# Kernel optimization log

Measured on AMD Instinct MI355X. Metric: run time of the kernel, lower is better.

Reference implementation:

```python
import jax, jax.numpy as jnp
import numpy as np

T_HORIZON, S_DIM, A_DIM, H = 65536, 128, 8, 256
GAMMA, LMBDA, EPS_CLIP, VF_COEF, ENT_COEF = 0.99, 0.95, 0.2, 0.5, 0.01
LOG2PI = float(np.log(2.0 * np.pi))


def setup_inputs() -> dict:
    key = jax.random.key(0)
    ks = jax.random.split(key, 24)
    s = jax.random.normal(ks[0], (T_HORIZON, S_DIM), jnp.float32)
    a = jax.random.normal(ks[1], (T_HORIZON, A_DIM), jnp.float32)
    r = jax.random.normal(ks[2], (T_HORIZON, 1), jnp.float32)
    sp = jax.random.normal(ks[3], (T_HORIZON, S_DIM), jnp.float32)
    log_prob_a_old = jax.random.normal(ks[4], (T_HORIZON, 1), jnp.float32)
    d_mask = (jax.random.uniform(ks[5], (T_HORIZON, 1)) > 0.05).astype(jnp.float32)

    def lin(k, fan_in, fan_out, std):
        return jax.random.normal(k, (fan_in, fan_out), jnp.float32) * (std / np.sqrt(fan_in))

    params = dict(
        pi_W1=lin(ks[6], S_DIM, H, np.sqrt(2)), pi_b1=jnp.zeros((H,), jnp.float32),
        pi_W2=lin(ks[7], H, H, np.sqrt(2)),     pi_b2=jnp.zeros((H,), jnp.float32),
        mu_W=lin(ks[8], H, A_DIM, 0.01),        mu_b=jnp.zeros((A_DIM,), jnp.float32),
        log_std=jnp.zeros((A_DIM,), jnp.float32),
        v_W1=lin(ks[9], S_DIM, H, np.sqrt(2)),  v_b1=jnp.zeros((H,), jnp.float32),
        v_W2=lin(ks[10], H, H, np.sqrt(2)),     v_b2=jnp.zeros((H,), jnp.float32),
        vh_W=lin(ks[11], H, 1, 1.0),            vh_b=jnp.zeros((1,), jnp.float32),
    )
    return dict(s=s, a=a, r=r, sp=sp, log_prob_a_old=log_prob_a_old, d_mask=d_mask, **params)


def reference(s, a, r, sp, log_prob_a_old, d_mask,
              pi_W1, pi_b1, pi_W2, pi_b2, mu_W, mu_b, log_std,
              v_W1, v_b1, v_W2, v_b2, vh_W, vh_b):
    def mlp(x, W1, b1, W2, b2):
        return jnp.tanh(jnp.tanh(x @ W1 + b1) @ W2 + b2)

    def v_fn(x):
        return mlp(x, v_W1, v_b1, v_W2, v_b2) @ vh_W + vh_b  # [N, 1]

    # ---- GAE (computed under no_grad in the original) ----
    values = jax.lax.stop_gradient(v_fn(s))                  # [T, 1]
    v_last = jax.lax.stop_gradient(v_fn(sp[-1:]))            # [1, 1]
    next_values = jnp.concatenate([values[1:], v_last], axis=0)
    deltas = r + GAMMA * next_values * d_mask - values       # [T, 1]

    def gae_step(gae, inp):
        delta, m = inp
        gae = delta + GAMMA * LMBDA * m * gae
        return gae, gae

    _, advantages = jax.lax.scan(gae_step, jnp.zeros((1,), deltas.dtype),
                                 (deltas, d_mask), reverse=True)  # [T, 1]
    returns = advantages + values
    advantages = (advantages - advantages.mean()) / (advantages.std(ddof=1) + 1e-8)
    advantages = jax.lax.stop_gradient(advantages)
    returns = jax.lax.stop_gradient(returns)

    # ---- PPO clipped loss (single full-batch pass) ----
    mu = mlp(s, pi_W1, pi_b1, pi_W2, pi_b2) @ mu_W + mu_b    # [T, A]
    std = jnp.exp(log_std)
    log_prob = (-0.5 * ((a - mu) / std) ** 2 - log_std - 0.5 * LOG2PI).sum(-1, keepdims=True)
    ratio = jnp.exp(log_prob - log_prob_a_old)               # [T, 1]
    pg_loss = -jnp.minimum(ratio * advantages,
                           jnp.clip(ratio, 1.0 - EPS_CLIP, 1.0 + EPS_CLIP) * advantages).mean()
    diff = v_fn(s) - returns
    vf_loss = jnp.where(jnp.abs(diff) < 1.0, 0.5 * diff ** 2, jnp.abs(diff) - 0.5).mean()
    entropy = (0.5 + 0.5 * LOG2PI + log_std).mean()          # Normal entropy, constant over batch
    return pg_loss + VF_COEF * vf_loss - ENT_COEF * entropy
```

## Files before the change

### kernel.cpp

```cpp
#include <hip/hip_runtime.h>
#include <math.h>

#define TH 65536
#define SD 128
#define AD 8
#define HD 256

constexpr float GAMMA  = 0.99f;
constexpr float LMBDA  = 0.95f;
constexpr float EPSC   = 0.2f;
constexpr float VFC    = 0.5f;
constexpr float ENTC   = 0.01f;
constexpr float LOG2PI = 1.8378770664093453f;

typedef _Float16 half8 __attribute__((ext_vector_type(8)));
typedef __fp16 fp16x2 __attribute__((ext_vector_type(2)));
typedef __attribute__((ext_vector_type(4))) float f32x4;

constexpr size_t WS_VALUES = 0;
constexpr size_t WS_RATIO  = 131080;
constexpr size_t WS_CHP    = 196616;
constexpr size_t WS_CHB    = 196680;
constexpr size_t WS_SCAL   = 196744;
constexpr size_t WS_BF     = 196752;
constexpr size_t SW_PIW1 = 0;
constexpr size_t SW_PIW2 = 32768;
constexpr size_t SW_VW1  = 98304;
constexpr size_t SW_VW2  = 131072;

__device__ __forceinline__ unsigned pk2h(float a, float b) {
    fp16x2 h = __builtin_amdgcn_cvt_pkrtz(a, b);
    return __builtin_bit_cast(unsigned, h);
}

__device__ __forceinline__ float ftanh(float x) {
    float cx = fminf(fmaxf(x, -9.f), 9.f);
    float e = __expf(cx + cx);
    return (e - 1.f) * __builtin_amdgcn_rcpf(e + 1.f);
}

__global__ __launch_bounds__(256) void swizzle_kernel(
    const float* __restrict__ piW1, const float* __restrict__ vW1,
    const float* __restrict__ piW2, const float* __restrict__ vW2,
    unsigned short* __restrict__ dPiW1, unsigned short* __restrict__ dVW1,
    unsigned short* __restrict__ dPiW2, unsigned short* __restrict__ dVW2,
    float* __restrict__ scal)
{
    if (blockIdx.x == 0 && threadIdx.x < 8) scal[threadIdx.x] = 0.f;
    int g = blockIdx.x * 256 + threadIdx.x;
    const float* S; unsigned short* D; int lo;
    if      (g <  8192) { S = piW1; D = dPiW1; lo = 0;     }
    else if (g < 24576) { S = piW2; D = dPiW2; lo = 8192;  }
    else if (g < 32768) { S = vW1;  D = dVW1;  lo = 24576; }
    else                { S = vW2;  D = dVW2;  lo = 32768; }
    int q = g - lo;
    int k = q >> 6, n4 = (q & 63) * 4;
    float4 v = *(const float4*)(S + (size_t)k * HD + n4);
    int ks = k >> 5, kq = (k >> 3) & 3, j = k & 7;
    int nt = n4 >> 4, nr = n4 & 15;
    unsigned short* base = D + ((size_t)(ks * 16 + nt) * 64 + kq * 16 + nr) * 8 + j;
    unsigned p01 = pk2h(v.x, v.y);
    unsigned p23 = pk2h(v.z, v.w);
    base[0]  = (unsigned short)(p01 & 0xffff);
    base[8]  = (unsigned short)(p01 >> 16);
    base[16] = (unsigned short)(p23 & 0xffff);
    base[24] = (unsigned short)(p23 >> 16);
}

__device__ __forceinline__ void runlayer1(
    f32x4* acc, const unsigned short* __restrict__ Ws,
    const half8* afr, int colhalf, int lane)
{
#pragma unroll
    for (int nt = 0; nt < 8; ++nt) acc[nt] = (f32x4){0.f, 0.f, 0.f, 0.f};
#pragma unroll
    for (int ks = 0; ks < 4; ++ks) {
#pragma unroll
        for (int ntl = 0; ntl < 8; ++ntl) {
            half8 bf = ((const half8*)Ws)[(ks * 16 + colhalf * 8 + ntl) * 64 + lane];
            acc[ntl] = __builtin_amdgcn_mfma_f32_16x16x32_f16(afr[ks], bf, acc[ntl], 0, 0, 0);
        }
    }
}

__device__ __forceinline__ void runlayer2(
    f32x4* acc, const unsigned short* __restrict__ Ws,
    const unsigned short* h1, int l15, int quad, int rowgrp, int colhalf, int lane)
{
#pragma unroll
    for (int nt = 0; nt < 8; ++nt) acc[nt] = (f32x4){0.f, 0.f, 0.f, 0.f};
#pragma unroll
    for (int ks = 0; ks < 8; ++ks) {
        half8 af = *(const half8*)(h1 + (rowgrp * 16 + l15) * 264 + ks * 32 + quad * 8);
#pragma unroll
        for (int ntl = 0; ntl < 8; ++ntl) {
            half8 bf = ((const half8*)Ws)[(ks * 16 + colhalf * 8 + ntl) * 64 + lane];
            acc[ntl] = __builtin_amdgcn_mfma_f32_16x16x32_f16(af, bf, acc[ntl], 0, 0, 0);
        }
    }
}

__device__ __forceinline__ void store4(unsigned short* dst, int stride,
                                       float t0, float t1, float t2, float t3)
{
    unsigned p01 = pk2h(t0, t1), p23 = pk2h(t2, t3);
    dst[0]          = (unsigned short)(p01 & 0xffff);
    dst[stride]     = (unsigned short)(p01 >> 16);
    dst[2 * stride] = (unsigned short)(p23 & 0xffff);
    dst[3 * stride] = (unsigned short)(p23 >> 16);
}

__global__ __launch_bounds__(256, 4) void mlp_fused_kernel(
    const float* __restrict__ X, const float* __restrict__ Xlast,
    const unsigned short* __restrict__ piW1s, const float* __restrict__ pib1,
    const unsigned short* __restrict__ piW2s, const float* __restrict__ pib2,
    const float* __restrict__ muW, const float* __restrict__ mub,
    const float* __restrict__ logstd,
    const float* __restrict__ act, const float* __restrict__ lpold,
    const unsigned short* __restrict__ vW1s, const float* __restrict__ vb1,
    const unsigned short* __restrict__ vW2s, const float* __restrict__ vb2,
    const float* __restrict__ vhW, const float* __restrict__ vhb,
    float* __restrict__ values, float* __restrict__ ratio)
{
    __shared__ unsigned short h1[32 * 264];
    __shared__ float cmb[32 * 8];
    __shared__ float val[32];
    const int tid = threadIdx.x;
    const int lane = tid & 63, wave = tid >> 6;
    const int l15 = lane & 15, quad = lane >> 4;
    const int rowgrp = wave >> 1, colhalf = wave & 1;
    const bool vonly = (blockIdx.x == gridDim.x - 1);
    const float* Xp = vonly ? Xlast : X + (size_t)blockIdx.x * 32 * SD;
    const int nrows = vonly ? 1 : 32;
    const int vout0 = vonly ? TH : blockIdx.x * 32;

    if (tid < 32) val[tid] = 0.f;
    cmb[tid] = 0.f;

    const int rr = rowgrp * 16 + l15;
    const float* xrow = Xp + (size_t)(rr < nrows ? rr : 0) * SD;
    half8 afr[4];
#pragma unroll
    for (int ks = 0; ks < 4; ++ks) {
        float4 v0 = *(const float4*)(xrow + ks * 32 + quad * 8);
        float4 v1 = *(const float4*)(xrow + ks * 32 + quad * 8 + 4);
        if (rr >= nrows) { v0 = make_float4(0.f, 0.f, 0.f, 0.f); v1 = v0; }
        uint4 u = make_uint4(pk2h(v0.x, v0.y), pk2h(v0.z, v0.w),
                             pk2h(v1.x, v1.y), pk2h(v1.z, v1.w));
        afr[ks] = __builtin_bit_cast(half8, u);
    }

    f32x4 acc[8];

    if (!vonly) {
        runlayer1(acc, piW1s, afr, colhalf, lane);
#pragma unroll
        for (int ntl = 0; ntl < 8; ++ntl) {
            int col = (colhalf * 8 + ntl) * 16 + l15;
            float bb = pib1[col];
            store4(&h1[(rowgrp * 16 + quad * 4) * 264 + col], 264,
                   ftanh(acc[ntl][0] + bb), ftanh(acc[ntl][1] + bb),
                   ftanh(acc[ntl][2] + bb), ftanh(acc[ntl][3] + bb));
        }
        __syncthreads();
        runlayer2(acc, piW2s, h1, l15, quad, rowgrp, colhalf, lane);
        float pm[4][8];
#pragma unroll
        for (int rg = 0; rg < 4; ++rg)
#pragma unroll
            for (int aj = 0; aj < 8; ++aj) pm[rg][aj] = 0.f;
#pragma unroll
        for (int ntl = 0; ntl < 8; ++ntl) {
            int col = (colhalf * 8 + ntl) * 16 + l15;
            float bb = pib2[col];
            float4 w0 = *(const float4*)(muW + (size_t)col * AD);
            float4 w1 = *(const float4*)(muW + (size_t)col * AD + 4);
            float wv[8] = {w0.x, w0.y, w0.z, w0.w, w1.x, w1.y, w1.z, w1.w};
#pragma unroll
            for (int rg = 0; rg < 4; ++rg) {
                float hv = ftanh(acc[ntl][rg] + bb);
#pragma unroll
                for (int aj = 0; aj < 8; ++aj) pm[rg][aj] = fmaf(hv, wv[aj], pm[rg][aj]);
            }
        }
#pragma unroll
        for (int off = 8; off >= 1; off >>= 1)
#pragma unroll
            for (int rg = 0; rg < 4; ++rg)
#pragma unroll
                for (int aj = 0; aj < 8; ++aj)
                    pm[rg][aj] += __shfl_xor(pm[rg][aj], off, 16);
        if (l15 == 0) {
#pragma unroll
            for (int rg = 0; rg < 4; ++rg) {
                int rowi = rowgrp * 16 + quad * 4 + rg;
#pragma unroll
                for (int aj = 0; aj < 8; ++aj)
                    atomicAdd(&cmb[rowi * 8 + aj], pm[rg][aj]);
            }
        }
        __syncthreads();
        if (tid < 32) {
            int row = blockIdx.x * 32 + tid;
            const float* ar = act + (size_t)row * AD;
            float lp = 0.f;
#pragma unroll
            for (int aj = 0; aj < 8; ++aj) {
                float ls = logstd[aj];
                float mu = cmb[tid * 8 + aj] + mub[aj];
                float z = (ar[aj] - mu) * __expf(-ls);
                lp += -0.5f * z * z - ls;
            }
            lp -= 4.f * LOG2PI;
            ratio[row] = __expf(lp - lpold[row]);
        }
        __syncthreads();
    }

    runlayer1(acc, vW1s, afr, colhalf, lane);
#pragma unroll
    for (int ntl = 0; ntl < 8; ++ntl) {
        int col = (colhalf * 8 + ntl) * 16 + l15;
        float bb = vb1[col];
        store4(&h1[(rowgrp * 16 + quad * 4) * 264 + col], 264,
               ftanh(acc[ntl][0] + bb), ftanh(acc[ntl][1] + bb),
               ftanh(acc[ntl][2] + bb), ftanh(acc[ntl][3] + bb));
    }
    __syncthreads();
    runlayer2(acc, vW2s, h1, l15, quad, rowgrp, colhalf, lane);
    float vp[4] = {0.f, 0.f, 0.f, 0.f};
#pragma unroll
    for (int ntl = 0; ntl < 8; ++ntl) {
        int col = (colhalf * 8 + ntl) * 16 + l15;
        float bb = vb2[col], w = vhW[col];
#pragma unroll
        for (int rg = 0; rg < 4; ++rg) vp[rg] += ftanh(acc[ntl][rg] + bb) * w;
    }
#pragma unroll
    for (int off = 8; off >= 1; off >>= 1)
#pragma unroll
        for (int rg = 0; rg < 4; ++rg) vp[rg] += __shfl_xor(vp[rg], off, 16);
    if (l15 == 0) {
#pragma unroll
        for (int rg = 0; rg < 4; ++rg)
            atomicAdd(&val[rowgrp * 16 + quad * 4 + rg], vp[rg]);
    }
    __syncthreads();
    if (tid < nrows)
        values[vout0 + tid] = val[tid] + vhb[0];
}

__global__ __launch_bounds__(256) void gae_fused_kernel(
    const float* __restrict__ rw, const float* __restrict__ m,
    const float* __restrict__ values, const float* __restrict__ ratio,
    const float* __restrict__ logstd,
    float* __restrict__ chunkP, float* __restrict__ chunkB,
    float* __restrict__ scal, float* __restrict__ out)
{
    __shared__ float sp_[256], sb_[256];
    __shared__ float cp[64], cb[64];
    __shared__ float red[12];
    __shared__ float bcast[4];
    const int j = threadIdx.x;
    const int t0 = blockIdx.x * 1024 + j * 4;
    const float g = GAMMA * LMBDA;

    float4 vv = *(const float4*)(values + t0);
    float v4 = values[t0 + 4];
    float4 rr = *(const float4*)(rw + t0);
    float4 mm = *(const float4*)(m + t0);
    float vs[5] = {vv.x, vv.y, vv.z, vv.w, v4};
    float rs[4] = {rr.x, rr.y, rr.z, rr.w};
    float ms[4] = {mm.x, mm.y, mm.z, mm.w};
    float ds[4];
#pragma unroll
    for (int i = 0; i < 4; ++i)
        ds[i] = rs[i] + GAMMA * vs[i + 1] * ms[i] - vs[i];

    float P = 1.f, B = 0.f;
#pragma unroll
    for (int i = 3; i >= 0; --i) {
        float p = g * ms[i];
        B = ds[i] + p * B;
        P = p * P;
    }
    sp_[j] = P; sb_[j] = B;
    __syncthreads();
    for (int dstep = 1; dstep < 256; dstep <<= 1) {
        float pj = sp_[j], bj = sb_[j], pk = 1.f, bk = 0.f;
        if (j + dstep < 256) { pk = sp_[j + dstep]; bk = sb_[j + dstep]; }
        __syncthreads();
        sp_[j] = pj * pk;
        sb_[j] = bj + pj * bk;
        __syncthreads();
    }
    if (j == 0) {
        atomicExch(&chunkP[blockIdx.x], sp_[0]);
        atomicExch(&chunkB[blockIdx.x], sb_[0]);
        __threadfence();
        atomicAdd(&scal[5], 1.f);
        while (atomicAdd(&scal[5], 0.f) < 64.f) __builtin_amdgcn_s_sleep(2);
    }
    __syncthreads();
    if (j < 64) {
        cp[j] = atomicAdd(&chunkP[j], 0.f);
        cb[j] = atomicAdd(&chunkB[j], 0.f);
    }
    __syncthreads();
    if (j == 0) {
        float A = 0.f;
        for (int c = 63; c > (int)blockIdx.x; --c) A = cb[c] + cp[c] * A;
        bcast[0] = A;
    }
    __syncthreads();
    const float carry = bcast[0];

    float Pe = 1.f, Be = 0.f;
    if (j < 255) { Pe = sp_[j + 1]; Be = sb_[j + 1]; }
    float A = Be + Pe * carry;
    float s1 = 0.f, s2 = 0.f, vf = 0.f;
    float a4[4];
#pragma unroll
    for (int i = 3; i >= 0; --i) {
        A = ds[i] + g * ms[i] * A;
        a4[i] = A;
        float ab = fabsf(A);
        vf += (ab < 1.f) ? 0.5f * A * A : ab - 0.5f;
        s1 += A;
        s2 += A * A;
    }
#pragma unroll
    for (int off = 32; off >= 1; off >>= 1) {
        s1 += __shfl_down(s1, off, 64);
        s2 += __shfl_down(s2, off, 64);
        vf += __shfl_down(vf, off, 64);
    }
    if ((j & 63) == 0) {
        int w = j >> 6;
        red[w] = s1; red[4 + w] = s2; red[8 + w] = vf;
    }
    __syncthreads();
    if (j == 0) {
        atomicAdd(&scal[0], red[0] + red[1] + red[2] + red[3]);
        atomicAdd(&scal[1], red[4] + red[5] + red[6] + red[7]);
        atomicAdd(&scal[2], red[8] + red[9] + red[10] + red[11]);
        __threadfence();
        atomicAdd(&scal[6], 1.f);
        while (atomicAdd(&scal[6], 0.f) < 64.f) __builtin_amdgcn_s_sleep(2);
        bcast[1] = atomicAdd(&scal[0], 0.f);
        bcast[2] = atomicAdd(&scal[1], 0.f);
    }
    __syncthreads();

    const float ssum = bcast[1], ssq = bcast[2];
    const float meanA = ssum / (float)TH;
    const float varA = fmaxf((ssq - ssum * ssum / (float)TH) / (float)(TH - 1), 0.f);
    const float inv = 1.f / (sqrtf(varA) + 1e-8f);

    float4 r4 = *(const float4*)(ratio + t0);
    float rt[4] = {r4.x, r4.y, r4.z, r4.w};
    float pg = 0.f;
#pragma unroll
    for (int i = 0; i < 4; ++i) {
        float aN = (a4[i] - meanA) * inv;
        float rc = fminf(fmaxf(rt[i], 1.f - EPSC), 1.f + EPSC);
        pg -= fminf(rt[i] * aN, rc * aN);
    }
#pragma unroll
    for (int off = 32; off >= 1; off >>= 1) pg += __shfl_down(pg, off, 64);
    if ((j & 63) == 0) red[j >> 6] = pg;
    __syncthreads();
    if (j == 0) {
        atomicAdd(&scal[3], red[0] + red[1] + red[2] + red[3]);
        __threadfence();
        float old = atomicAdd(&scal[4], 1.f);
        if (old == 63.f) {
            float pgs = atomicAdd(&scal[3], 0.f);
            float vfs = atomicAdd(&scal[2], 0.f);
            float ls = 0.f;
#pragma unroll
            for (int jj = 0; jj < AD; ++jj) ls += logstd[jj];
            float entropy = 0.5f + 0.5f * LOG2PI + ls / (float)AD;
            out[0] = pgs / (float)TH + VFC * (vfs / (float)TH) - ENTC * entropy;
        }
    }
}

extern "C" void kernel_launch(void* const* d_in, const int* in_sizes, int n_in,
                              void* d_out, int out_size, void* d_ws, size_t ws_size,
                              hipStream_t stream) {
    const float* s      = (const float*)d_in[0];
    const float* a      = (const float*)d_in[1];
    const float* r      = (const float*)d_in[2];
    const float* sp     = (const float*)d_in[3];
    const float* lpold  = (const float*)d_in[4];
    const float* dmask  = (const float*)d_in[5];
    const float* piW1   = (const float*)d_in[6];
    const float* pib1   = (const float*)d_in[7];
    const float* piW2   = (const float*)d_in[8];
    const float* pib2   = (const float*)d_in[9];
    const float* muW    = (const float*)d_in[10];
    const float* mub    = (const float*)d_in[11];
    const float* logstd = (const float*)d_in[12];
    const float* vW1    = (const float*)d_in[13];
    const float* vb1    = (const float*)d_in[14];
    const float* vW2    = (const float*)d_in[15];
    const float* vb2    = (const float*)d_in[16];
    const float* vhW    = (const float*)d_in[17];
    const float* vhb    = (const float*)d_in[18];

    float* ws      = (float*)d_ws;
    float* values  = ws + WS_VALUES;
    float* ratio   = ws + WS_RATIO;
    float* chunkP  = ws + WS_CHP;
    float* chunkB  = ws + WS_CHB;
    float* scal    = ws + WS_SCAL;
    unsigned short* bfbase = (unsigned short*)(ws + WS_BF);
    unsigned short* dPiW1 = bfbase + SW_PIW1;
    unsigned short* dPiW2 = bfbase + SW_PIW2;
    unsigned short* dVW1  = bfbase + SW_VW1;
    unsigned short* dVW2  = bfbase + SW_VW2;

    swizzle_kernel<<<192, 256, 0, stream>>>(piW1, vW1, piW2, vW2,
                                            dPiW1, dVW1, dPiW2, dVW2, scal);

    mlp_fused_kernel<<<TH / 32 + 1, 256, 0, stream>>>(
        s, sp + (size_t)(TH - 1) * SD,
        dPiW1, pib1, dPiW2, pib2, muW, mub, logstd, a, lpold,
        dVW1, vb1, dVW2, vb2, vhW, vhb,
        values, ratio);

    gae_fused_kernel<<<64, 256, 0, stream>>>(r, dmask, values, ratio, logstd,
                                             chunkP, chunkB, scal, (float*)d_out);
}
```

Measured before the change: 211.0 us.

## Run policy and value MLPs concurrently in 512-thread blocks; cheaper tanh and polling

The MLP kernel now launches 512 threads per block, with waves 0-3 computing the policy network and waves 4-7 the value network at the same time, each using its own shared h1 buffer. Before, one set of waves ran both networks one after the other with extra barriers. This cuts the serial per-block chain and the number of __syncthreads. It also drops the clamp in tanh and rewrites it as 1-2/(e+1), and replaces the atomicAdd(…,0) spin reads with relaxed atomic loads plus a longer sleep. The cost is more shared memory and registers per block under launch_bounds(512,4), which may lower occupancy.

```diff
diff --git a/kernel.cpp b/kernel.cpp
--- a/kernel.cpp
+++ b/kernel.cpp
@@ -34,9 +34,12 @@
 }
 
 __device__ __forceinline__ float ftanh(float x) {
-    float cx = fminf(fmaxf(x, -9.f), 9.f);
-    float e = __expf(cx + cx);
-    return (e - 1.f) * __builtin_amdgcn_rcpf(e + 1.f);
+    float e = __expf(x + x);
+    return fmaf(-2.f, __builtin_amdgcn_rcpf(e + 1.f), 1.f);
+}
+
+__device__ __forceinline__ float atomLoad(const float* p) {
+    return __hip_atomic_load(p, __ATOMIC_RELAXED, __HIP_MEMORY_SCOPE_AGENT);
 }
 
 __global__ __launch_bounds__(256) void swizzle_kernel(
@@ -67,6 +70,21 @@
     base[24] = (unsigned short)(p23 >> 16);
 }
 
+__device__ __forceinline__ void loadA(half8* afr, const float* __restrict__ Xp,
+                                      int rr, int nrows, int quad)
+{
+    const float* xrow = Xp + (size_t)(rr < nrows ? rr : 0) * SD;
+#pragma unroll
+    for (int ks = 0; ks < 4; ++ks) {
+        float4 v0 = *(const float4*)(xrow + ks * 32 + quad * 8);
+        float4 v1 = *(const float4*)(xrow + ks * 32 + quad * 8 + 4);
+        if (rr >= nrows) { v0 = make_float4(0.f, 0.f, 0.f, 0.f); v1 = v0; }
+        uint4 u = make_uint4(pk2h(v0.x, v0.y), pk2h(v0.z, v0.w),
+                             pk2h(v1.x, v1.y), pk2h(v1.z, v1.w));
+        afr[ks] = __builtin_bit_cast(half8, u);
+    }
+}
+
 __device__ __forceinline__ void runlayer1(
     f32x4* acc, const unsigned short* __restrict__ Ws,
     const half8* afr, int colhalf, int lane)
@@ -110,7 +128,7 @@
     dst[3 * stride] = (unsigned short)(p23 >> 16);
 }
 
-__global__ __launch_bounds__(256, 4) void mlp_fused_kernel(
+__global__ __launch_bounds__(512, 4) void mlp_fused_kernel(
     const float* __restrict__ X, const float* __restrict__ Xlast,
     const unsigned short* __restrict__ piW1s, const float* __restrict__ pib1,
     const unsigned short* __restrict__ piW2s, const float* __restrict__ pib2,
@@ -122,48 +140,45 @@
     const float* __restrict__ vhW, const float* __restrict__ vhb,
     float* __restrict__ values, float* __restrict__ ratio)
 {
-    __shared__ unsigned short h1[32 * 264];
+    __shared__ unsigned short h1[2][32 * 264];
     __shared__ float cmb[32 * 8];
     __shared__ float val[32];
     const int tid = threadIdx.x;
     const int lane = tid & 63, wave = tid >> 6;
     const int l15 = lane & 15, quad = lane >> 4;
-    const int rowgrp = wave >> 1, colhalf = wave & 1;
+    const int net = wave >> 2;
+    const int rowgrp = (wave >> 1) & 1, colhalf = wave & 1;
     const bool vonly = (blockIdx.x == gridDim.x - 1);
     const float* Xp = vonly ? Xlast : X + (size_t)blockIdx.x * 32 * SD;
     const int nrows = vonly ? 1 : 32;
     const int vout0 = vonly ? TH : blockIdx.x * 32;
 
+    const unsigned short* W1s = net ? vW1s : piW1s;
+    const unsigned short* W2s = net ? vW2s : piW2s;
+    const float* b1 = net ? vb1 : pib1;
+
     if (tid < 32) val[tid] = 0.f;
-    cmb[tid] = 0.f;
-
-    const int rr = rowgrp * 16 + l15;
-    const float* xrow = Xp + (size_t)(rr < nrows ? rr : 0) * SD;
+    if (tid < 256) cmb[tid] = 0.f;
+
     half8 afr[4];
-#pragma unroll
-    for (int ks = 0; ks < 4; ++ks) {
-        float4 v0 = *(const float4*)(xrow + ks * 32 + quad * 8);
-        float4 v1 = *(const float4*)(xrow + ks * 32 + quad * 8 + 4);
-        if (rr >= nrows) { v0 = make_float4(0.f, 0.f, 0.f, 0.f); v1 = v0; }
-        uint4 u = make_uint4(pk2h(v0.x, v0.y), pk2h(v0.z, v0.w),
-                             pk2h(v1.x, v1.y), pk2h(v1.z, v1.w));
-        afr[ks] = __builtin_bit_cast(half8, u);
-    }
+    loadA(afr, Xp, rowgrp * 16 + l15, nrows, quad);
 
     f32x4 acc[8];
 
-    if (!vonly) {
-        runlayer1(acc, piW1s, afr, colhalf, lane);
-#pragma unroll
-        for (int ntl = 0; ntl < 8; ++ntl) {
-            int col = (colhalf * 8 + ntl) * 16 + l15;
-            float bb = pib1[col];
-            store4(&h1[(rowgrp * 16 + quad * 4) * 264 + col], 264,
-                   ftanh(acc[ntl][0] + bb), ftanh(acc[ntl][1] + bb),
-                   ftanh(acc[ntl][2] + bb), ftanh(acc[ntl][3] + bb));
-        }
-        __syncthreads();
-        runlayer2(acc, piW2s, h1, l15, quad, rowgrp, colhalf, lane);
+    runlayer1(acc, W1s, afr, colhalf, lane);
+#pragma unroll
+    for (int ntl = 0; ntl < 8; ++ntl) {
+        int col = (colhalf * 8 + ntl) * 16 + l15;
+        float bb = b1[col];
+        store4(&h1[net][(rowgrp * 16 + quad * 4) * 264 + col], 264,
+               ftanh(acc[ntl][0] + bb), ftanh(acc[ntl][1] + bb),
+               ftanh(acc[ntl][2] + bb), ftanh(acc[ntl][3] + bb));
+    }
+    __syncthreads();
+
+    runlayer2(acc, W2s, h1[net], l15, quad, rowgrp, colhalf, lane);
+
+    if (net == 0) {
         float pm[4][8];
 #pragma unroll
         for (int rg = 0; rg < 4; ++rg)
@@ -199,53 +214,41 @@
                     atomicAdd(&cmb[rowi * 8 + aj], pm[rg][aj]);
             }
         }
-        __syncthreads();
-        if (tid < 32) {
-            int row = blockIdx.x * 32 + tid;
-            const float* ar = act + (size_t)row * AD;
-            float lp = 0.f;
-#pragma unroll
-            for (int aj = 0; aj < 8; ++aj) {
-                float ls = logstd[aj];
-                float mu = cmb[tid * 8 + aj] + mub[aj];
-                float z = (ar[aj] - mu) * __expf(-ls);
-                lp += -0.5f * z * z - ls;
-            }
-            lp -= 4.f * LOG2PI;
-            ratio[row] = __expf(lp - lpold[row]);
-        }
-        __syncthreads();
-    }
-
-    runlayer1(acc, vW1s, afr, colhalf, lane);
-#pragma unroll
-    for (int ntl = 0; ntl < 8; ++ntl) {
-        int col = (colhalf * 8 + ntl) * 16 + l15;
-        float bb = vb1[col];
-        store4(&h1[(rowgrp * 16 + quad * 4) * 264 + col], 264,
-               ftanh(acc[ntl][0] + bb), ftanh(acc[ntl][1] + bb),
-               ftanh(acc[ntl][2] + bb), ftanh(acc[ntl][3] + bb));
-    }
-    __syncthreads();
-    runlayer2(acc, vW2s, h1, l15, quad, rowgrp, colhalf, lane);
-    float vp[4] = {0.f, 0.f, 0.f, 0.f};
-#pragma unroll
-    for (int ntl = 0; ntl < 8; ++ntl) {
-        int col = (colhalf * 8 + ntl) * 16 + l15;
-        float bb = vb2[col], w = vhW[col];
-#pragma unroll
-        for (int rg = 0; rg < 4; ++rg) vp[rg] += ftanh(acc[ntl][rg] + bb) * w;
-    }
-#pragma unroll
-    for (int off = 8; off >= 1; off >>= 1)
-#pragma unroll
-        for (int rg = 0; rg < 4; ++rg) vp[rg] += __shfl_xor(vp[rg], off, 16);
-    if (l15 == 0) {
-#pragma unroll
-        for (int rg = 0; rg < 4; ++rg)
-            atomicAdd(&val[rowgrp * 16 + quad * 4 + rg], vp[rg]);
-    }
-    __syncthreads();
+    } else {
+        float vp[4] = {0.f, 0.f, 0.f, 0.f};
+#pragma unroll
+        for (int ntl = 0; ntl < 8; ++ntl) {
+            int col = (colhalf * 8 + ntl) * 16 + l15;
+            float bb = vb2[col], w = vhW[col];
+#pragma unroll
+            for (int rg = 0; rg < 4; ++rg) vp[rg] += ftanh(acc[ntl][rg] + bb) * w;
+        }
+#pragma unroll
+        for (int off = 8; off >= 1; off >>= 1)
+#pragma unroll
+            for (int rg = 0; rg < 4; ++rg) vp[rg] += __shfl_xor(vp[rg], off, 16);
+        if (l15 == 0) {
+#pragma unroll
+            for (int rg = 0; rg < 4; ++rg)
+                atomicAdd(&val[rowgrp * 16 + quad * 4 + rg], vp[rg]);
+        }
+    }
+    __syncthreads();
+
+    if (!vonly && tid < 32) {
+        int row = blockIdx.x * 32 + tid;
+        const float* ar = act + (size_t)row * AD;
+        float lp = 0.f;
+#pragma unroll
+        for (int aj = 0; aj < 8; ++aj) {
+            float ls = logstd[aj];
+            float mu = cmb[tid * 8 + aj] + mub[aj];
+            float z = (ar[aj] - mu) * __expf(-ls);
+            lp += -0.5f * z * z - ls;
+        }
+        lp -= 4.f * LOG2PI;
+        ratio[row] = __expf(lp - lpold[row]);
+    }
     if (tid < nrows)
         values[vout0 + tid] = val[tid] + vhb[0];
 }
@@ -299,12 +302,13 @@
         atomicExch(&chunkB[blockIdx.x], sb_[0]);
         __threadfence();
         atomicAdd(&scal[5], 1.f);
-        while (atomicAdd(&scal[5], 0.f) < 64.f) __builtin_amdgcn_s_sleep(2);
+        while (atomLoad(&scal[5]) < 64.f) __builtin_amdgcn_s_sleep(8);
+        __threadfence();
     }
     __syncthreads();
     if (j < 64) {
-        cp[j] = atomicAdd(&chunkP[j], 0.f);
-        cb[j] = atomicAdd(&chunkB[j], 0.f);
+        cp[j] = atomLoad(&chunkP[j]);
+        cb[j] = atomLoad(&chunkB[j]);
     }
     __syncthreads();
     if (j == 0) {
@@ -346,9 +350,10 @@
         atomicAdd(&scal[2], red[8] + red[9] + red[10] + red[11]);
         __threadfence();
         atomicAdd(&scal[6], 1.f);
-        while (atomicAdd(&scal[6], 0.f) < 64.f) __builtin_amdgcn_s_sleep(2);
-        bcast[1] = atomicAdd(&scal[0], 0.f);
-        bcast[2] = atomicAdd(&scal[1], 0.f);
+        while (atomLoad(&scal[6]) < 64.f) __builtin_amdgcn_s_sleep(8);
+        __threadfence();
+        bcast[1] = atomLoad(&scal[0]);
+        bcast[2] = atomLoad(&scal[1]);
     }
     __syncthreads();
 
@@ -375,8 +380,8 @@
         __threadfence();
         float old = atomicAdd(&scal[4], 1.f);
         if (old == 63.f) {
-            float pgs = atomicAdd(&scal[3], 0.f);
-            float vfs = atomicAdd(&scal[2], 0.f);
+            float pgs = atomLoad(&scal[3]);
+            float vfs = atomLoad(&scal[2]);
             float ls = 0.f;
 #pragma unroll
             for (int jj = 0; jj < AD; ++jj) ls += logstd[jj];
@@ -424,7 +429,7 @@
     swizzle_kernel<<<192, 256, 0, stream>>>(piW1, vW1, piW2, vW2,
                                             dPiW1, dVW1, dPiW2, dVW2, scal);
 
-    mlp_fused_kernel<<<TH / 32 + 1, 256, 0, stream>>>(
+    mlp_fused_kernel<<<TH / 32 + 1, 512, 0, stream>>>(
         s, sp + (size_t)(TH - 1) * SD,
         dPiW1, pib1, dPiW2, pib2, muW, mub, logstd, a, lpold,
         dVW1, vb1, dVW2, vb2, vhW, vhb,
```

Measured after the change: 224.4 us. 6.3% more time.
